# Performance work log

Hardware: AMD Instinct MI355X
Metric: run time of the kernel (lower is better)

Reference implementation:

```python
import jax, jax.numpy as jnp
import numpy as np

D_MODEL = 512
N_HEADS = 8
HEAD_DIM = D_MODEL // N_HEADS
ROPE_BASE = 10000.0


def _rope_cache(seq_len, dtype):
    half = HEAD_DIM // 2
    inv_freq = 1.0 / (ROPE_BASE ** (jnp.arange(half, dtype=dtype) / half))
    t = jnp.arange(seq_len, dtype=dtype)
    freqs = jnp.einsum('i,j->ij', t, inv_freq)            # [L, half]
    cos = jnp.repeat(jnp.cos(freqs), 2, axis=-1)          # [L, head_dim]
    sin = jnp.repeat(jnp.sin(freqs), 2, axis=-1)
    return cos[None, None], sin[None, None]               # [1,1,L,head_dim]


def _rotate_half(x):
    x_even = x[..., ::2]
    x_odd = x[..., 1::2]
    return jnp.stack([-x_odd, x_even], axis=-1).reshape(x.shape)


def setup_inputs() -> dict:
    key = jax.random.key(0)
    ks = jax.random.split(key, 10)
    B, Lq, Lkv, C = 2, 2048, 4096, D_MODEL
    s = 1.0 / np.sqrt(C)
    inp = {
        'q': jax.random.normal(ks[0], (B, Lq, C), jnp.float32),
        'kv': jax.random.normal(ks[1], (B, Lkv, C), jnp.float32),
        'Wq': jax.random.normal(ks[2], (C, C), jnp.float32) * s,
        'bq': jnp.zeros((C,), jnp.float32),
        'Wk': jax.random.normal(ks[3], (C, C), jnp.float32) * s,
        'bk': jnp.zeros((C,), jnp.float32),
        'Wv': jax.random.normal(ks[4], (C, C), jnp.float32) * s,
        'bv': jnp.zeros((C,), jnp.float32),
        'Wo': jax.random.normal(ks[5], (C, C), jnp.float32) * s,
        'bo': jnp.zeros((C,), jnp.float32),
    }
    return inp


def reference(q, kv, Wq, bq, Wk, bk, Wv, bv, Wo, bo):
    B, Lq, C = q.shape
    Lkv = kv.shape[1]
    H, Dh = N_HEADS, HEAD_DIM
    # projections (torch Linear: x @ W.T + b)
    qh = (q @ Wq.T + bq).reshape(B, Lq, H, Dh).transpose(0, 2, 1, 3)    # [B,H,Lq,Dh]
    kh = (kv @ Wk.T + bk).reshape(B, Lkv, H, Dh).transpose(0, 2, 1, 3)  # [B,H,Lkv,Dh]
    vh = (kv @ Wv.T + bv).reshape(B, Lkv, H, Dh).transpose(0, 2, 1, 3)
    # RoPE applied to K only
    cos, sin = _rope_cache(Lkv, kh.dtype)
    kh = kh * cos + _rotate_half(kh) * sin
    # manual softmax attention (full [B,H,Lq,Lkv] matrix, as in the source)
    scale = 1.0 / np.sqrt(Dh).astype(np.float32)
    attn = jnp.einsum('bhqd,bhkd->bhqk', qh, kh) * scale
    attn = jax.nn.softmax(attn, axis=-1)
    out = jnp.einsum('bhqk,bhkd->bhqd', attn, vh)
    out = out.transpose(0, 2, 1, 3).reshape(B, Lq, C)
    return out @ Wo.T + bo
```

## Files before the change

### kernel.cpp

```cpp
#include <hip/hip_runtime.h>
#include <math.h>

typedef _Float16 f16;
typedef __attribute__((ext_vector_type(8))) f16 f16x8;
typedef __attribute__((ext_vector_type(4))) float f32x4;
typedef __attribute__((ext_vector_type(4))) int   i32x4;

__device__ __forceinline__ short f2h(float f) {
    return __builtin_bit_cast(short, (f16)f);
}
__device__ __forceinline__ float h2f(short s) {
    return (float)__builtin_bit_cast(f16, s);
}

__device__ __forceinline__ void gload16(const void* g, void* l) {
    __builtin_amdgcn_global_load_lds(
        (const __attribute__((address_space(1))) unsigned int*)g,
        (__attribute__((address_space(3))) unsigned int*)l, 16, 0, 0);
}

#define MFMA16(A, B, C) __builtin_amdgcn_mfma_f32_16x16x32_f16(A, B, C, 0, 0, 0)
#define EXP2(x) __builtin_amdgcn_exp2f(x)

__global__ __launch_bounds__(256) void convert_kernel(
    const float* __restrict__ q, const float* __restrict__ kv,
    const float* __restrict__ Wq, const float* __restrict__ Wk,
    const float* __restrict__ Wv, const float* __restrict__ Wo,
    short* __restrict__ cq, short* __restrict__ ckv,
    short* __restrict__ wq, short* __restrict__ wk,
    short* __restrict__ wv, short* __restrict__ wo)
{
    int g = blockIdx.x * 256 + threadIdx.x;
    const float* src; short* dst; int local;
    if      (g <  524288) { src = q;  dst = cq;  local = g; }
    else if (g < 1572864) { src = kv; dst = ckv; local = g -  524288; }
    else if (g < 1638400) { src = Wq; dst = wq;  local = g - 1572864; }
    else if (g < 1703936) { src = Wk; dst = wk;  local = g - 1638400; }
    else if (g < 1769472) { src = Wv; dst = wv;  local = g - 1703936; }
    else                  { src = Wo; dst = wo;  local = g - 1769472; }
    float4 v = *(const float4*)(src + (size_t)local * 4);
    short4 hv; short* hp = (short*)&hv;
    hp[0] = f2h(v.x); hp[1] = f2h(v.y); hp[2] = f2h(v.z); hp[3] = f2h(v.w);
    *(short4*)(dst + (size_t)local * 4) = hv;
}

template<int RT, int EP>
__device__ __forceinline__ void gemm_core(
    short* As, short* Bs,
    const short* __restrict__ X, const short* __restrict__ W,
    const float* __restrict__ bias, float scale,
    float* __restrict__ outF, short* __restrict__ outH,
    int m0, int n0)
{
    const int tid  = threadIdx.x;
    const int wave = tid >> 6, lane = tid & 63;
    const int quad = lane >> 4, col = lane & 15;
    const int wy = wave >> 1, wx = wave & 1;
    constexpr int MT  = RT / 32;
    constexpr int ASZ = RT * 32;

    f32x4 acc[MT][4];
    #pragma unroll
    for (int i = 0; i < MT; ++i)
        #pragma unroll
        for (int j = 0; j < 4; ++j) acc[i][j] = (f32x4){0.f, 0.f, 0.f, 0.f};

    int aoff[MT], boff[4];
    #pragma unroll
    for (int t = 0; t < MT; ++t)
        aoff[t] = (wy * (RT / 2) + t * 16 + col) * 32 + quad * 8;
    #pragma unroll
    for (int t = 0; t < 4; ++t)
        boff[t] = (wx * 64 + t * 16 + col) * 32 + quad * 8;

    const short* Abase = X + (size_t)m0 * 512;
    const short* Bbase = W + (size_t)n0 * 512;

#define STAGE_G(BUF, KB) {                                                   \
    _Pragma("unroll")                                                        \
    for (int i = 0; i < RT / 64; ++i) {                                      \
        int p = i * 256 + tid; int r = p >> 2, qq = p & 3;                   \
        gload16(Abase + (size_t)r * 512 + (KB) + qq * 8,                     \
                &As[(BUF) * ASZ + (i * 256 + wave * 64) * 8]);               \
    }                                                                        \
    _Pragma("unroll")                                                        \
    for (int i = 0; i < 2; ++i) {                                            \
        int p = i * 256 + tid; int r = p >> 2, qq = p & 3;                   \
        gload16(Bbase + (size_t)r * 512 + (KB) + qq * 8,                     \
                &Bs[(BUF) * 4096 + (i * 256 + wave * 64) * 8]);              \
    }                                                                        \
}

    STAGE_G(0, 0);
    asm volatile("s_waitcnt vmcnt(0)" ::: "memory");
    __syncthreads();

    for (int kb = 0; kb < 512; kb += 32) {
        const int cur = (kb >> 5) & 1;
        if (kb + 32 < 512) STAGE_G(cur ^ 1, kb + 32);
        f16x8 a[MT], b[4];
        #pragma unroll
        for (int t = 0; t < MT; ++t) a[t] = *(const f16x8*)&As[cur * ASZ + aoff[t]];
        #pragma unroll
        for (int t = 0; t < 4; ++t)  b[t] = *(const f16x8*)&Bs[cur * 4096 + boff[t]];
        #pragma unroll
        for (int tm = 0; tm < MT; ++tm)
            #pragma unroll
            for (int tn = 0; tn < 4; ++tn)
                acc[tm][tn] = MFMA16(a[tm], b[tn], acc[tm][tn]);
        asm volatile("s_waitcnt vmcnt(0)" ::: "memory");
        __syncthreads();
    }
#undef STAGE_G

    #pragma unroll
    for (int tn = 0; tn < 4; ++tn) {
        int ng = n0 + wx * 64 + tn * 16 + col;
        float bb = bias[ng];
        #pragma unroll
        for (int tm = 0; tm < MT; ++tm) {
            int mb = m0 + wy * (RT / 2) + tm * 16 + quad * 4;
            if constexpr (EP == 2) {
                int bb_ = mb >> 12, kvg = mb & 4095;
                int tile = kvg >> 7, kv128 = kvg & 127;
                int t01 = (kv128 >> 6) & 1, sv = (kv128 >> 4) & 3, qd = (kv128 >> 2) & 3;
                int hh = ng >> 6, dd = ng & 63, dt = dd >> 4, d15 = dd & 15;
                size_t base = ((((size_t)((bb_ * 8 + hh) * 32 + tile) * 16)
                               + sv * 4 + dt) * 64 + qd * 16 + d15) * 8 + t01 * 4;
                short4 s4; short* sp = (short*)&s4;
                #pragma unroll
                for (int r = 0; r < 4; ++r) sp[r] = f2h(acc[tm][tn][r] + bb);
                *(short4*)&outH[base] = s4;
            } else if constexpr (EP == 1) {
                #pragma unroll
                for (int r = 0; r < 4; ++r)
                    outH[(size_t)(mb + r) * 512 + ng] =
                        f2h((acc[tm][tn][r] + bb) * scale);
            } else {
                #pragma unroll
                for (int r = 0; r < 4; ++r)
                    outF[(size_t)(mb + r) * 512 + ng] = acc[tm][tn][r] + bb;
            }
        }
    }
}

__global__ __launch_bounds__(256) void fused_qkv_gemm_kernel(
    const short* __restrict__ cq, const short* __restrict__ ckv,
    const short* __restrict__ wq, const short* __restrict__ wk,
    const short* __restrict__ wv,
    const float* __restrict__ bq, const float* __restrict__ bk,
    const float* __restrict__ bv, float qscale,
    short* __restrict__ Qh, short* __restrict__ Kh, short* __restrict__ Vf)
{
    __shared__ short As[2 * 128 * 32], Bs[2 * 128 * 32];
    int bi = blockIdx.x;
    if (bi < 128) {
        gemm_core<128, 1>(As, Bs, cq, wq, bq, qscale, nullptr, Qh,
                          (bi >> 2) * 128, (bi & 3) * 128);
    } else if (bi < 384) {
        bi -= 128;
        gemm_core<128, 1>(As, Bs, ckv, wk, bk, 1.0f, nullptr, Kh,
                          (bi >> 2) * 128, (bi & 3) * 128);
    } else {
        bi -= 384;
        gemm_core<128, 2>(As, Bs, ckv, wv, bv, 1.0f, nullptr, Vf,
                          (bi >> 2) * 128, (bi & 3) * 128);
    }
}

__global__ __launch_bounds__(256) void gemm_o_kernel(
    const short* __restrict__ X, const short* __restrict__ W,
    const float* __restrict__ bias, float* __restrict__ outF)
{
    __shared__ short As[2 * 64 * 32], Bs[2 * 128 * 32];
    gemm_core<64, 0>(As, Bs, X, W, bias, 1.0f, outF, nullptr,
                     (int)(blockIdx.x >> 2) * 64, (int)(blockIdx.x & 3) * 128);
}

__global__ __launch_bounds__(256) void rope_kernel(short* __restrict__ Kh)
{
    __shared__ float2 tbl[4][32];
    const int t = threadIdx.x;
    const int g = blockIdx.x * 256 + t;
    if (t < 128) {
        int p = t >> 5, i = t & 31;
        int pos = (blockIdx.x * 4 + p) & 4095;
        float fr = expf((float)i * -0.28782313662425576f);
        float sv, cv;
        sincosf((float)pos * fr, &sv, &cv);
        tbl[p][i] = make_float2(cv, sv);
    }
    __syncthreads();

    int row = g >> 6;
    int c8  = (g & 63) * 8;
    size_t off = (size_t)row * 512 + c8;
    f16x8 hv = *(const f16x8*)&Kh[off];
    float x[8];
    #pragma unroll
    for (int j = 0; j < 8; ++j) x[j] = (float)hv[j];
    const int rl = row & 3;
    const int ib = (c8 & 63) >> 1;
    #pragma unroll
    for (int p = 0; p < 4; ++p) {
        float2 cs = tbl[rl][ib + p];
        float e = x[2 * p], o = x[2 * p + 1];
        x[2 * p]     = e * cs.x - o * cs.y;
        x[2 * p + 1] = o * cs.x + e * cs.y;
    }
    #pragma unroll
    for (int j = 0; j < 8; ++j) hv[j] = (f16)x[j];
    *(f16x8*)&Kh[off] = hv;
}

__global__ __launch_bounds__(256, 2) void attn_mfma_kernel(
    const short* __restrict__ Qh, const short* __restrict__ Kh,
    const short* __restrict__ Vfrag, short* __restrict__ AO)
{
    __shared__ char smem[34816];

    const int tid  = threadIdx.x;
    const int wave = tid >> 6;
    const int lane = tid & 63;
    const int quad = lane >> 4;
    const int l15  = lane & 15;

    const int bh = blockIdx.x & 15;
    const int qt = blockIdx.x >> 4;
    const int b  = bh >> 3, h = bh & 7;
    const int qb = qt * 64;

    f16x8 qf[4][2];
    #pragma unroll
    for (int tq = 0; tq < 4; ++tq)
        #pragma unroll
        for (int c = 0; c < 2; ++c)
            qf[tq][c] = *(const f16x8*)&Qh[((size_t)(b * 2048 + qb + tq * 16 + l15)) * 512
                                           + h * 64 + c * 32 + quad * 8];

    f32x4 o[4][4];
    f32x4 l4[4];
    #pragma unroll
    for (int i = 0; i < 4; ++i) {
        l4[i] = (f32x4){0.f, 0.f, 0.f, 0.f};
        #pragma unroll
        for (int j = 0; j < 4; ++j) o[i][j] = (f32x4){0.f, 0.f, 0.f, 0.f};
    }

    const f32x4 zero4 = (f32x4){0.f, 0.f, 0.f, 0.f};
    f16x8 vones;
    #pragma unroll
    for (int j = 0; j < 8; ++j) vones[j] = (f16)1.0f;

    const short* kp = Kh + ((size_t)(b * 4096 + wave * 16 + l15)) * 512
                      + h * 64 + quad * 8;
    const short* vbase = Vfrag + (size_t)(b * 8 + h) * 262144
                         + ((size_t)(wave * 4) * 64 + lane) * 8;

#define LDK(DST, I) { const short* _k = kp + (size_t)(I) * 65536;            \
    DST[0] = *(const f16x8*)(_k);                                            \
    DST[1] = *(const f16x8*)(_k + 32);                                       \
    DST[2] = *(const f16x8*)(_k + 32768);                                    \
    DST[3] = *(const f16x8*)(_k + 32800); }
#define LDV(DST, I) { const short* _v = vbase + (size_t)(I) * 8192;          \
    DST[0] = *(const f16x8*)(_v);                                            \
    DST[1] = *(const f16x8*)(_v + 512);                                      \
    DST[2] = *(const f16x8*)(_v + 1024);                                     \
    DST[3] = *(const f16x8*)(_v + 1536); }

#define QK(KC) {                                                             \
    __builtin_amdgcn_s_setprio(1);                                           \
    _Pragma("unroll")                                                        \
    for (int t = 0; t < 4; ++t) {                                            \
        s0[t] = MFMA16(KC[0], qf[t][0], zero4);                              \
        s0[t] = MFMA16(KC[1], qf[t][1], s0[t]);                              \
        s1[t] = MFMA16(KC[2], qf[t][0], zero4);                              \
        s1[t] = MFMA16(KC[3], qf[t][1], s1[t]);                              \
    }                                                                        \
    __builtin_amdgcn_s_setprio(0); }

#define FIN(VP) {                                                            \
    _Pragma("unroll")                                                        \
    for (int t = 0; t < 4; ++t) {                                            \
        float e0 = EXP2(s0[t][0]), e1 = EXP2(s0[t][1]);                      \
        float e2 = EXP2(s0[t][2]), e3 = EXP2(s0[t][3]);                      \
        float e4 = EXP2(s1[t][0]), e5 = EXP2(s1[t][1]);                      \
        float e6 = EXP2(s1[t][2]), e7 = EXP2(s1[t][3]);                      \
        i32x4 pw;                                                            \
        pw.x = __builtin_bit_cast(int, __builtin_amdgcn_cvt_pkrtz(e0, e1));  \
        pw.y = __builtin_bit_cast(int, __builtin_amdgcn_cvt_pkrtz(e2, e3));  \
        pw.z = __builtin_bit_cast(int, __builtin_amdgcn_cvt_pkrtz(e4, e5));  \
        pw.w = __builtin_bit_cast(int, __builtin_amdgcn_cvt_pkrtz(e6, e7));  \
        f16x8 p8 = __builtin_bit_cast(f16x8, pw);                            \
        __builtin_amdgcn_s_setprio(1);                                       \
        _Pragma("unroll")                                                    \
        for (int dt = 0; dt < 4; ++dt)                                       \
            o[t][dt] = MFMA16(p8, VP[dt], o[t][dt]);                         \
        l4[t] = MFMA16(p8, vones, l4[t]);                                    \
        __builtin_amdgcn_s_setprio(0);                                       \
    } }

#define BODY(I, KC, KN, VP) {                                                \
    LDK(KN, (I) + 1);                                                        \
    FIN(VP);                                                                 \
    LDV(VP, (I) + 1);                                                        \
    QK(KC); }

    f16x8 kA[4], kB[4], vA[4], vB[4];
    f32x4 s0[4], s1[4];

    LDK(kA, 0); LDV(vA, 0); LDK(kB, 1); LDV(vB, 1);
    QK(kA);

    #pragma unroll 1
    for (int j = 1; j < 31; j += 2) {
        BODY(j,     kB, kA, vA);
        BODY(j + 1, kA, kB, vB);
    }
    BODY(31, kB, kA, vA);
    FIN(vB);

#undef BODY
#undef FIN
#undef QK
#undef LDV
#undef LDK

    float* Opart = (float*)smem;
    float* Lpart = (float*)(smem + 33792);

    float inv_save[8];
    #pragma unroll
    for (int pass = 0; pass < 2; ++pass) {
        if (pass) __syncthreads();
        #pragma unroll
        for (int tq = 0; tq < 4; ++tq)
            #pragma unroll
            for (int dh = 0; dh < 2; ++dh) {
                int dt = pass * 2 + dh;
                #pragma unroll
                for (int r = 0; r < 4; ++r)
                    Opart[wave * (64 * 33) + (tq * 16 + quad * 4 + r) * 33 + dh * 16 + l15] = o[tq][dt][r];
            }
        if (pass == 0 && l15 == 0) {
            #pragma unroll
            for (int tq = 0; tq < 4; ++tq)
                #pragma unroll
                for (int r = 0; r < 4; ++r)
                    Lpart[wave * 64 + tq * 16 + quad * 4 + r] = l4[tq][r];
        }
        __syncthreads();
        #pragma unroll
        for (int r = 0; r < 8; ++r) {
            int qq = wave * 16 + r * 2 + (lane >> 5);
            int d  = lane & 31;
            float v = Opart[0 * (64 * 33) + qq * 33 + d] + Opart[1 * (64 * 33) + qq * 33 + d]
                    + Opart[2 * (64 * 33) + qq * 33 + d] + Opart[3 * (64 * 33) + qq * 33 + d];
            float inv;
            if (pass == 0) {
                float l = Lpart[qq] + Lpart[64 + qq] + Lpart[128 + qq] + Lpart[192 + qq];
                inv = 1.0f / l;
                inv_save[r] = inv;
            } else {
                inv = inv_save[r];
            }
            float val = v * inv;
            size_t oo = ((size_t)(b * 2048 + qb + qq)) * 512 + h * 64 + pass * 32 + d;
            AO[oo] = f2h(val);
        }
    }
}

extern "C" void kernel_launch(void* const* d_in, const int* in_sizes, int n_in,
                              void* d_out, int out_size, void* d_ws, size_t ws_size,
                              hipStream_t stream) {
    const float* q  = (const float*)d_in[0];
    const float* kv = (const float*)d_in[1];
    const float* Wq = (const float*)d_in[2];
    const float* bq = (const float*)d_in[3];
    const float* Wk = (const float*)d_in[4];
    const float* bk = (const float*)d_in[5];
    const float* Wv = (const float*)d_in[6];
    const float* bv = (const float*)d_in[7];
    const float* Wo = (const float*)d_in[8];
    const float* bo = (const float*)d_in[9];
    float* out = (float*)d_out;

    char* ws = (char*)d_ws;
    const size_t MB = 1024 * 1024;
    short* cq  = (short*)(ws + 0 * MB);
    short* ckv = (short*)(ws + 4 * MB);
    short* wq  = (short*)(ws + 12 * MB);
    short* wk  = wq + 262144;
    short* wv  = wk + 262144;
    short* wo  = wv + 262144;
    short* Qh  = (short*)(ws + 14 * MB);
    short* Kh  = (short*)(ws + 18 * MB);
    short* Vf  = (short*)(ws + 26 * MB);
    short* AO  = (short*)(ws + 34 * MB);

    const float qscale = 0.18033688011112043f;

    dim3 blk(256);
    convert_kernel<<<7168, blk, 0, stream>>>(
        q, kv, Wq, Wk, Wv, Wo, cq, ckv, wq, wk, wv, wo);

    fused_qkv_gemm_kernel<<<640, blk, 0, stream>>>(
        cq, ckv, wq, wk, wv, bq, bk, bv, qscale, Qh, Kh, Vf);

    rope_kernel<<<2048, blk, 0, stream>>>(Kh);

    attn_mfma_kernel<<<512, blk, 0, stream>>>(Qh, Kh, Vf, AO);

    gemm_o_kernel<<<256, blk, 0, stream>>>(AO, wo, bo, out);
}
```

Baseline: 166.1 us.

## Split attention KV range in two and add partial-sum reduce kernel

The attention kernel now processes half of the KV sequence per block, doubling the grid, and writes unnormalized fp32 partial outputs and row sums to workspace. A new reduce kernel adds the two halves, divides by the combined denominator, and emits fp16 attention output. This aims to raise parallelism and shorten per-block loops, at the cost of extra global memory traffic for the fp32 partials and an additional kernel launch.

```diff
diff --git a/kernel.cpp b/kernel.cpp
--- a/kernel.cpp
+++ b/kernel.cpp
@@ -8,9 +8,6 @@
 
 __device__ __forceinline__ short f2h(float f) {
     return __builtin_bit_cast(short, (f16)f);
-}
-__device__ __forceinline__ float h2f(short s) {
-    return (float)__builtin_bit_cast(f16, s);
 }
 
 __device__ __forceinline__ void gload16(const void* g, void* l) {
@@ -216,7 +213,8 @@
 
 __global__ __launch_bounds__(256, 2) void attn_mfma_kernel(
     const short* __restrict__ Qh, const short* __restrict__ Kh,
-    const short* __restrict__ Vfrag, short* __restrict__ AO)
+    const short* __restrict__ Vfrag,
+    float* __restrict__ Opar, float* __restrict__ Lpar)
 {
     __shared__ char smem[34816];
 
@@ -226,8 +224,9 @@
     const int quad = lane >> 4;
     const int l15  = lane & 15;
 
-    const int bh = blockIdx.x & 15;
-    const int qt = blockIdx.x >> 4;
+    const int bh   = blockIdx.x & 15;
+    const int qt   = (blockIdx.x >> 4) & 31;
+    const int half = blockIdx.x >> 9;
     const int b  = bh >> 3, h = bh & 7;
     const int qb = qt * 64;
 
@@ -253,9 +252,10 @@
     #pragma unroll
     for (int j = 0; j < 8; ++j) vones[j] = (f16)1.0f;
 
-    const short* kp = Kh + ((size_t)(b * 4096 + wave * 16 + l15)) * 512
+    const short* kp = Kh + ((size_t)(b * 4096 + half * 2048 + wave * 16 + l15)) * 512
                       + h * 64 + quad * 8;
     const short* vbase = Vfrag + (size_t)(b * 8 + h) * 262144
+                         + (size_t)half * 131072
                          + ((size_t)(wave * 4) * 64 + lane) * 8;
 
 #define LDK(DST, I) { const short* _k = kp + (size_t)(I) * 65536;            \
@@ -314,11 +314,11 @@
     QK(kA);
 
     #pragma unroll 1
-    for (int j = 1; j < 31; j += 2) {
+    for (int j = 1; j < 15; j += 2) {
         BODY(j,     kB, kA, vA);
         BODY(j + 1, kA, kB, vB);
     }
-    BODY(31, kB, kA, vA);
+    BODY(15, kB, kA, vA);
     FIN(vB);
 
 #undef BODY
@@ -329,8 +329,9 @@
 
     float* Opart = (float*)smem;
     float* Lpart = (float*)(smem + 33792);
-
-    float inv_save[8];
+    float* Oh = Opar + (size_t)half * 2097152;
+    float* Lh = Lpar + (size_t)half * 32768;
+
     #pragma unroll
     for (int pass = 0; pass < 2; ++pass) {
         if (pass) __syncthreads();
@@ -357,19 +358,33 @@
             int d  = lane & 31;
             float v = Opart[0 * (64 * 33) + qq * 33 + d] + Opart[1 * (64 * 33) + qq * 33 + d]
                     + Opart[2 * (64 * 33) + qq * 33 + d] + Opart[3 * (64 * 33) + qq * 33 + d];
-            float inv;
-            if (pass == 0) {
+            size_t row = (size_t)(b * 2048 + qb + qq);
+            if (pass == 0 && d == 0) {
                 float l = Lpart[qq] + Lpart[64 + qq] + Lpart[128 + qq] + Lpart[192 + qq];
-                inv = 1.0f / l;
-                inv_save[r] = inv;
-            } else {
-                inv = inv_save[r];
+                Lh[row * 8 + h] = l;
             }
-            float val = v * inv;
-            size_t oo = ((size_t)(b * 2048 + qb + qq)) * 512 + h * 64 + pass * 32 + d;
-            AO[oo] = f2h(val);
+            Oh[row * 512 + h * 64 + pass * 32 + d] = v;
         }
     }
+}
+
+__global__ __launch_bounds__(256) void attn_reduce_kernel(
+    const float* __restrict__ Opar, const float* __restrict__ Lpar,
+    short* __restrict__ AO)
+{
+    int base = (blockIdx.x * 256 + threadIdx.x) * 4;
+    int row = base >> 9;
+    int col = base & 511;
+    float4 o0 = *(const float4*)&Opar[base];
+    float4 o1 = *(const float4*)&Opar[2097152 + base];
+    int lidx = row * 8 + (col >> 6);
+    float inv = 1.0f / (Lpar[lidx] + Lpar[32768 + lidx]);
+    short4 out;
+    out.x = f2h((o0.x + o1.x) * inv);
+    out.y = f2h((o0.y + o1.y) * inv);
+    out.z = f2h((o0.z + o1.z) * inv);
+    out.w = f2h((o0.w + o1.w) * inv);
+    *(short4*)&AO[base] = out;
 }
 
 extern "C" void kernel_launch(void* const* d_in, const int* in_sizes, int n_in,
@@ -399,6 +414,8 @@
     short* Kh  = (short*)(ws + 18 * MB);
     short* Vf  = (short*)(ws + 26 * MB);
     short* AO  = (short*)(ws + 34 * MB);
+    float* Opar = (float*)(ws + 38 * MB);
+    float* Lpar = (float*)(ws + 54 * MB);
 
     const float qscale = 0.18033688011112043f;
 
@@ -411,7 +428,9 @@
 
     rope_kernel<<<2048, blk, 0, stream>>>(Kh);
 
-    attn_mfma_kernel<<<512, blk, 0, stream>>>(Qh, Kh, Vf, AO);
+    attn_mfma_kernel<<<1024, blk, 0, stream>>>(Qh, Kh, Vf, Opar, Lpar);
+
+    attn_reduce_kernel<<<2048, blk, 0, stream>>>(Opar, Lpar, AO);
 
     gemm_o_kernel<<<256, blk, 0, stream>>>(AO, wo, bo, out);
 }
```

Measured after the change: 174.2 us. +4.9%, slower.
